# Kernel optimization log

Hardware: AMD Instinct MI355X
Metric: run time of the kernel (lower is better)

The kernel has to match this reference:

```python
import jax, jax.numpy as jnp
import numpy as np

NH = 8          # num_heads
NEG = -1e30     # mask_logits fill value


def setup_inputs() -> dict:
    key = jax.random.key(0)
    k1, k2, k3, k4 = jax.random.split(key, 4)
    B, D, T = 4, 1024, 2048
    x = jax.random.normal(k1, (B, D, T), dtype=jnp.float32)
    mask = jax.random.randint(k2, (B, T), 0, 2).astype(jnp.float32)
    # xavier-uniform-ish linear weights, torch layout [out, in]
    lim = float(np.sqrt(6.0 / (D + D)))
    Wq = jax.random.uniform(k3, (D, D), dtype=jnp.float32, minval=-lim, maxval=lim)
    Wo = jax.random.uniform(k4, (D, D), dtype=jnp.float32, minval=-lim, maxval=lim)
    return {"x": x, "mask": mask, "Wq": Wq, "Wo": Wo}


def reference(x, mask, Wq, Wo):
    # x: [B, D, T] channels-first; mask: [B, T] in {0,1} float
    B, D, T = x.shape
    dk = D // NH
    scale = 1.0 / jnp.sqrt(jnp.asarray(dk, x.dtype))
    xt = jnp.transpose(x, (0, 2, 1))                 # [B, T, D]
    # NOTE: original source uses Wqs for Q, K and V (source bug, reproduced)
    q = xt @ Wq.T                                    # [B, T, D]
    qh = q.reshape(B, T, NH, dk).transpose(0, 2, 1, 3)  # [B, H, T, dk]
    scores = scale * jnp.einsum('bhqd,bhkd->bhqk', qh, qh)  # [B, H, T, T]
    cmask = mask[:, None, None, :]                   # column mask [B,1,1,T]
    rmask = mask[:, None, :, None]                   # row mask    [B,1,T,1]
    logits = (scores * cmask + (1.0 - cmask) * NEG) * rmask
    attn = jax.nn.softmax(logits, axis=-1)
    ctx = jnp.einsum('bhqk,bhkd->bhqd', attn, qh)    # [B, H, T, dk]
    ctx = ctx.transpose(0, 2, 1, 3).reshape(B, T, D)
    out = ctx @ Wo.T                                 # [B, T, D]
    return jnp.transpose(out, (0, 2, 1))             # [B, D, T]
```

## Files before the change

### kernel.cpp

```cpp
#include <hip/hip_runtime.h>

#define TT 2048
#define DD 1024
#define NHH 8
#define DKK 128
#define SCALE2 0.1275174724f

typedef __attribute__((ext_vector_type(8)))  short short8;
typedef __attribute__((ext_vector_type(4)))  short short4v;
typedef __attribute__((ext_vector_type(4)))  float float4v;
typedef __attribute__((ext_vector_type(16))) float float16v;
typedef __attribute__((ext_vector_type(4)))  int   int4v;

__device__ __forceinline__ short f2bf(float f) {
  union { float f; unsigned u; } v; v.f = f;
  unsigned r = v.u + 0x7FFFu + ((v.u >> 16) & 1u);
  return (short)(r >> 16);
}
__device__ __forceinline__ unsigned cvtpk(float lo, float hi) {
  unsigned r;
  asm("v_cvt_pk_bf16_f32 %0, %1, %2" : "=v"(r) : "v"(lo), "v"(hi));
  return r;
}
__device__ __forceinline__ float xhalf_add(float x) {
  float y;
  asm("v_mov_b32 %0, %1" : "=v"(y) : "v"(x));
  asm("v_permlane32_swap_b32 %0, %1" : "+v"(x), "+v"(y));
  return x + y;
}
__device__ __forceinline__ int s4(int row) {
  return (row & 7) ^ (((row >> 3) & 3) << 2);
}
__device__ __forceinline__ void gl2lds(const void* g, void* l) {
  __builtin_amdgcn_global_load_lds(
      (const __attribute__((address_space(1))) void*)g,
      (__attribute__((address_space(3))) void*)l, 16, 0, 0);
}

__global__ __launch_bounds__(256) void k_prep(const float* __restrict__ x,
                                              short* __restrict__ xt,
                                              const float* __restrict__ Wq,
                                              short* __restrict__ wqb,
                                              const float* __restrict__ Wo,
                                              short* __restrict__ wob) {
  int id = blockIdx.x;
  if (id < 8192) {
    __shared__ float tile[32][33];
    int ttile = id & 63, dtile = (id >> 6) & 31, b = id >> 11;
    int d0 = dtile << 5, t0 = ttile << 5;
    int tx = threadIdx.x & 31, ty = threadIdx.x >> 5;
    const float* xp = x + ((size_t)b * DD + d0) * TT + t0;
#pragma unroll
    for (int yy = 0; yy < 32; yy += 8)
      tile[ty + yy][tx] = xp[(size_t)(ty + yy) * TT + tx];
    __syncthreads();
    short* op = xt + ((size_t)b * TT + t0) * DD + d0;
#pragma unroll
    for (int yy = 0; yy < 32; yy += 8)
      op[(size_t)(ty + yy) * DD + tx] = f2bf(tile[tx][ty + yy]);
  } else {
    const float* w = (id < 9216) ? Wq : Wo;
    short* o = (id < 9216) ? wqb : wob;
    int i = (id - 8192 - ((id < 9216) ? 0 : 1024)) * 256 + threadIdx.x;
    float4v v = ((const float4v*)w)[i];
    short4v s;
#pragma unroll
    for (int j = 0; j < 4; ++j) s[j] = f2bf(v[j]);
    ((short4v*)o)[i] = s;
  }
}

template <int EPI>
__global__ __launch_bounds__(256) void k_gemm(const short* __restrict__ A,
                                              const short* __restrict__ Bt,
                                              void* __restrict__ Cout,
                                              short* __restrict__ qhT) {
  __shared__ __align__(16) short As[128 * 64];
  __shared__ __align__(16) short Bs[128 * 64];
  __shared__ __align__(16) short Ct[(EPI == 0) ? 128 * 136 : 1];
  const int K = 1024;
  int tm = blockIdx.x * 128, tn = blockIdx.y * 128;
  int tid = threadIdx.x, lane = tid & 63, w = tid >> 6;
  int wm = (w >> 1) * 64, wn = (w & 1) * 64;
  int ql = lane & 15, g = lane >> 4;

  int srow[4], scol[4];
#pragma unroll
  for (int c = 0; c < 4; ++c) {
    int cg = w * 4 + c;
    int r = cg * 8 + (lane >> 3);
    srow[c] = r;
    scol[c] = ((lane & 7) ^ (r & 7)) * 8;
  }

  float4v acc[4][4];
#pragma unroll
  for (int mt = 0; mt < 4; ++mt)
#pragma unroll
    for (int nt = 0; nt < 4; ++nt) acc[mt][nt] = (float4v){0.f, 0.f, 0.f, 0.f};

  for (int k0 = 0; k0 < K; k0 += 64) {
    __syncthreads();
#pragma unroll
    for (int c = 0; c < 4; ++c) {
      int cg = w * 4 + c;
      gl2lds(A + (size_t)(tm + srow[c]) * K + k0 + scol[c], As + cg * 512);
      gl2lds(Bt + (size_t)(tn + srow[c]) * K + k0 + scol[c], Bs + cg * 512);
    }
    __syncthreads();
#pragma unroll
    for (int k4 = 0; k4 < 2; ++k4) {
      short8 af[4], bfr[4];
#pragma unroll
      for (int mt = 0; mt < 4; ++mt) {
        int row = wm + mt * 16 + ql;
        af[mt] = *(const short8*)(As + row * 64 + (((k4 * 4 + g) ^ (ql & 7)) * 8));
      }
#pragma unroll
      for (int nt = 0; nt < 4; ++nt) {
        int row = wn + nt * 16 + ql;
        bfr[nt] = *(const short8*)(Bs + row * 64 + (((k4 * 4 + g) ^ (ql & 7)) * 8));
      }
#pragma unroll
      for (int mt = 0; mt < 4; ++mt)
#pragma unroll
        for (int nt = 0; nt < 4; ++nt)
          acc[mt][nt] = __builtin_amdgcn_mfma_f32_16x16x32_bf16(af[mt], bfr[nt],
                                                                acc[mt][nt], 0, 0, 0);
    }
  }

  if (EPI == 1) {
#pragma unroll
    for (int mt = 0; mt < 4; ++mt)
#pragma unroll
      for (int nt = 0; nt < 4; ++nt)
#pragma unroll
        for (int r = 0; r < 4; ++r) {
          int m = tm + wm + mt * 16 + g * 4 + r;
          int n = tn + wn + nt * 16 + ql;
          int b = n >> 11, t = n & 2047;
          ((float*)Cout)[((size_t)b * 1024 + m) * 2048 + t] = acc[mt][nt][r];
        }
  } else {
    __syncthreads();
#pragma unroll
    for (int mt = 0; mt < 4; ++mt)
#pragma unroll
      for (int nt = 0; nt < 4; ++nt)
#pragma unroll
        for (int r = 0; r < 4; ++r)
          Ct[(wm + mt * 16 + g * 4 + r) * 136 + wn + nt * 16 + ql] =
              f2bf(acc[mt][nt][r]);
    __syncthreads();
    int bb = tm >> 11, t0 = tm & 2047;
    short* qb = (short*)Cout;
    {
      int m = tid >> 1, c0 = (tid & 1) * 64;
      short* dst = qb + (size_t)(tm + m) * 1024 + tn + c0;
      const short* src = Ct + m * 136 + c0;
#pragma unroll
      for (int i = 0; i < 8; ++i)
        *(short8*)(dst + i * 8) = *(const short8*)(src + i * 8);
    }
    {
      int n = tid >> 1, m0 = (tid & 1) * 64;
      short* dst = qhT + ((size_t)(bb * DD + tn + n)) * TT + t0 + m0;
#pragma unroll
      for (int i = 0; i < 8; ++i) {
        short8 v;
#pragma unroll
        for (int j = 0; j < 8; ++j) v[j] = Ct[(m0 + i * 8 + j) * 136 + n];
        *(short8*)(dst + i * 8) = v;
      }
    }
  }
}

__global__ __launch_bounds__(256, 2) void k_attn(const short* __restrict__ q,
                                                 const short* __restrict__ qhT,
                                                 const float* __restrict__ mask,
                                                 short* __restrict__ ctx) {
  __shared__ __align__(16) short Ks[2][64 * 128];
  __shared__ __align__(16) short Vt[2][128 * 64];
  __shared__ __align__(16) short Kx[2][64 * 16];

  int bh = blockIdx.x, qt = blockIdx.y;
  int b = bh >> 3, h = bh & 7;
  int tid = threadIdx.x, lane = tid & 63, w = tid >> 6;
  int ql32 = lane & 31, hi = lane >> 5;
  int csw = s4(ql32);
  int vsw = ql32 & 7;
  short negbig = f2bf(-1e30f);

  int qrow = qt * 128 + w * 32 + ql32;
  const short* qp = q + ((size_t)(b * TT + qrow)) * DD + h * DKK;
  short8 qf[8];
#pragma unroll
  for (int kc8 = 0; kc8 < 8; ++kc8)
    qf[kc8] = *(const short8*)(qp + kc8 * 16 + hi * 8);
  float rm = mask[(size_t)b * TT + qrow];

  float qs = SCALE2 * rm;
#pragma unroll
  for (int kc8 = 0; kc8 < 8; ++kc8) {
    union { short8 s; unsigned u[4]; } a;
    a.s = qf[kc8];
#pragma unroll
    for (int j = 0; j < 4; ++j) {
      union { unsigned u; float f; } lo, hh;
      lo.u = a.u[j] << 16;
      hh.u = a.u[j] & 0xFFFF0000u;
      a.u[j] = cvtpk(lo.f * qs, hh.f * qs);
    }
    qf[kc8] = a.s;
  }
  short8 bext = (short8)0;
  if (hi == 0) bext[0] = (rm != 0.f) ? (short)0x3F80 : (short)0;

  int oc = tid & 15, r2 = tid >> 4;
  const short* kbase_g = q + ((size_t)b * TT) * DD + h * DKK + oc * 8;
  const short* vbase_g = qhT + ((size_t)(b * DD + h * DKK)) * TT;
  int vd[4], vko[4], vwoff[4];
#pragma unroll
  for (int p = 0; p < 4; ++p) {
    int idx = p * 256 + tid;
    vd[p] = idx >> 3;
    vko[p] = idx & 7;
    vwoff[p] = vd[p] * 64 + ((vko[p] ^ (vd[p] & 7)) * 8);
  }
  int kwoff[2][2];
#pragma unroll
  for (int ps = 0; ps < 2; ++ps) {
    int ra = 2 * r2 + 32 * ps, rb = ra + 1;
    kwoff[ps][0] = ra * 128 + ((oc ^ s4(ra)) * 8);
    kwoff[ps][1] = rb * 128 + ((oc ^ s4(rb)) * 8);
  }

  short8 va[2], vb[2], vv[4];
#pragma unroll
  for (int ps = 0; ps < 2; ++ps) {
    const short* kp = kbase_g + (size_t)(2 * r2 + 32 * ps) * DD;
    va[ps] = *(const short8*)(kp);
    vb[ps] = *(const short8*)(kp + DD);
  }
#pragma unroll
  for (int p = 0; p < 4; ++p)
    vv[p] = *(const short8*)(vbase_g + (size_t)vd[p] * TT + vko[p] * 8);
  float mreg = mask[(size_t)b * TT + lane];

#pragma unroll
  for (int ps = 0; ps < 2; ++ps) {
    *(short8*)(Ks[0] + kwoff[ps][0]) = va[ps];
    *(short8*)(Ks[0] + kwoff[ps][1]) = vb[ps];
  }
#pragma unroll
  for (int p = 0; p < 4; ++p)
    *(short8*)(Vt[0] + vwoff[p]) = vv[p];
  if (tid < 128) {
    short8 z = (short8)0;
    if (tid < 64) z[0] = (mreg != 0.f) ? (short)0 : negbig;
    *(short8*)(&Kx[0][0] + tid * 16) = z;
    *(short8*)(&Kx[0][0] + tid * 16 + 8) = (short8)0;
  }

  float l_run = 0.f;
  float16v o[4];
#pragma unroll
  for (int nt = 0; nt < 4; ++nt)
#pragma unroll
    for (int r = 0; r < 16; ++r) o[nt][r] = 0.f;

  for (int kt = 0; kt < 32; ++kt) {
    int cur = kt & 1;
    const short* ksb = Ks[cur];
    const short* vtb = Vt[cur];
    const short* kxb = Kx[cur];
    short* ksn = Ks[cur ^ 1];
    short* vtn = Vt[cur ^ 1];
    short* kxn = Kx[cur ^ 1];

    __syncthreads();

    if (kt < 31) {
      int kb0n = (kt + 1) * 64;
      const short* kpn = kbase_g + (size_t)kb0n * DD;
#pragma unroll
      for (int ps = 0; ps < 2; ++ps) {
        const short* kp = kpn + (size_t)(2 * r2 + 32 * ps) * DD;
        va[ps] = *(const short8*)(kp);
        vb[ps] = *(const short8*)(kp + DD);
      }
#pragma unroll
      for (int p = 0; p < 4; ++p)
        vv[p] = *(const short8*)(vbase_g + (size_t)vd[p] * TT + kb0n + vko[p] * 8);
      mreg = mask[(size_t)b * TT + kb0n + lane];
    }

    float16v st0, st1;
#pragma unroll
    for (int r = 0; r < 16; ++r) { st0[r] = 0.f; st1[r] = 0.f; }
    __builtin_amdgcn_s_setprio(1);
    {
      short8 ax0 = *(const short8*)(kxb + ql32 * 16 + hi * 8);
      short8 ax1 = *(const short8*)(kxb + (32 + ql32) * 16 + hi * 8);
      st0 = __builtin_amdgcn_mfma_f32_32x32x16_bf16(ax0, bext, st0, 0, 0, 0);
      st1 = __builtin_amdgcn_mfma_f32_32x32x16_bf16(ax1, bext, st1, 0, 0, 0);
    }
#pragma unroll
    for (int kc8 = 0; kc8 < 8; ++kc8) {
      int csk = ((kc8 * 2 + hi) ^ csw) * 8;
      short8 kf0 = *(const short8*)(ksb + ql32 * 128 + csk);
      short8 kf1 = *(const short8*)(ksb + (32 + ql32) * 128 + csk);
      st0 = __builtin_amdgcn_mfma_f32_32x32x16_bf16(kf0, qf[kc8], st0, 0, 0, 0);
      st1 = __builtin_amdgcn_mfma_f32_32x32x16_bf16(kf1, qf[kc8], st1, 0, 0, 0);
    }
    __builtin_amdgcn_s_setprio(0);

    float tsum = 0.f;
#pragma unroll
    for (int r = 0; r < 16; ++r) {
      float p0 = __builtin_amdgcn_exp2f(st0[r]);
      float p1 = __builtin_amdgcn_exp2f(st1[r]);
      st0[r] = p0; st1[r] = p1;
      tsum += p0 + p1;
    }
    l_run += xhalf_add(tsum);

    short8 pa[4];
#pragma unroll
    for (int kc = 0; kc < 4; ++kc) {
      int a0 = 2 * (kc & 1);
      unsigned x0, x1, y0, y1;
      if (kc < 2) {
        x0 = cvtpk(st0[4 * a0 + 0], st0[4 * a0 + 1]);
        x1 = cvtpk(st0[4 * a0 + 2], st0[4 * a0 + 3]);
        y0 = cvtpk(st0[4 * a0 + 4], st0[4 * a0 + 5]);
        y1 = cvtpk(st0[4 * a0 + 6], st0[4 * a0 + 7]);
      } else {
        x0 = cvtpk(st1[4 * a0 + 0], st1[4 * a0 + 1]);
        x1 = cvtpk(st1[4 * a0 + 2], st1[4 * a0 + 3]);
        y0 = cvtpk(st1[4 * a0 + 4], st1[4 * a0 + 5]);
        y1 = cvtpk(st1[4 * a0 + 6], st1[4 * a0 + 7]);
      }
      asm("v_permlane32_swap_b32 %0, %1" : "+v"(x0), "+v"(y0));
      asm("v_permlane32_swap_b32 %0, %1" : "+v"(x1), "+v"(y1));
      union { unsigned u[4]; short8 s8; } pu;
      pu.u[0] = x0; pu.u[1] = x1; pu.u[2] = y0; pu.u[3] = y1;
      pa[kc] = pu.s8;
    }

    __builtin_amdgcn_s_setprio(1);
#pragma unroll
    for (int nt = 0; nt < 4; ++nt) {
      int row = nt * 32 + ql32;
#pragma unroll
      for (int kc = 0; kc < 4; ++kc) {
        short8 vf = *(const short8*)(vtb + row * 64 + (((kc * 2 + hi) ^ vsw) * 8));
        o[nt] = __builtin_amdgcn_mfma_f32_32x32x16_bf16(vf, pa[kc], o[nt], 0, 0, 0);
      }
    }
    __builtin_amdgcn_s_setprio(0);

    if (kt < 31) {
#pragma unroll
      for (int ps = 0; ps < 2; ++ps) {
        *(short8*)(ksn + kwoff[ps][0]) = va[ps];
        *(short8*)(ksn + kwoff[ps][1]) = vb[ps];
      }
#pragma unroll
      for (int p = 0; p < 4; ++p)
        *(short8*)(vtn + vwoff[p]) = vv[p];
      if (tid < 64) {
        unsigned word = (mreg != 0.f) ? 0u : (unsigned)(unsigned short)negbig;
        *(unsigned*)(kxn + tid * 16) = word;
      }
    }
  }

  float il = 1.0f / l_run;
  short* cp = ctx + ((size_t)(b * TT + qrow)) * DD + h * DKK;
#pragma unroll
  for (int nt = 0; nt < 4; ++nt)
#pragma unroll
    for (int a = 0; a < 4; ++a) {
      short4v sv;
#pragma unroll
      for (int j = 0; j < 4; ++j) sv[j] = f2bf(o[nt][4 * a + j] * il);
      *(short4v*)(cp + nt * 32 + 8 * a + 4 * hi) = sv;
    }
}

extern "C" void kernel_launch(void* const* d_in, const int* in_sizes, int n_in,
                              void* d_out, int out_size, void* d_ws, size_t ws_size,
                              hipStream_t stream) {
  const float* x    = (const float*)d_in[0];
  const float* mask = (const float*)d_in[1];
  const float* Wq   = (const float*)d_in[2];
  const float* Wo   = (const float*)d_in[3];
  char* ws = (char*)d_ws;
  short* xt  = (short*)(ws);
  short* wqb = (short*)(ws + (size_t)16 * 1024 * 1024);
  short* wob = (short*)(ws + (size_t)18 * 1024 * 1024);
  short* qb  = (short*)(ws + (size_t)20 * 1024 * 1024);
  short* ctx = (short*)(ws + (size_t)36 * 1024 * 1024);
  short* qhT = (short*)(ws + (size_t)52 * 1024 * 1024);

  k_prep<<<10240, 256, 0, stream>>>(x, xt, Wq, wqb, Wo, wob);
  k_gemm<0><<<dim3(64, 8), 256, 0, stream>>>(xt, wqb, qb, qhT);
  k_attn<<<dim3(32, 16), 256, 0, stream>>>(qb, qhT, mask, ctx);
  k_gemm<1><<<dim3(8, 64), 256, 0, stream>>>(wob, ctx, d_out, nullptr);
}
```

Baseline: 145.7 us.

## Split attention KV range across two wave groups per block and merge partials

The attention kernel now launches 512 threads per block, split into two 256-thread groups. Each group handles half of the key/value sequence for the same 128 query rows, and the two partial outputs and row sums are merged through shared memory at the end. The LDS double-buffering is replaced by single buffers per group with two barriers per iteration. The goal is more waves in flight, since the grid of 512 blocks underfills the device, at the cost of extra synchronization, a shared-memory reduction, and possibly lower occupancy from the larger LDS footprint and register pressure.

```diff
diff --git a/kernel.cpp b/kernel.cpp
--- a/kernel.cpp
+++ b/kernel.cpp
@@ -177,23 +177,34 @@
   }
 }
 
-__global__ __launch_bounds__(256, 2) void k_attn(const short* __restrict__ q,
+__global__ __launch_bounds__(512, 4) void k_attn(const short* __restrict__ q,
                                                  const short* __restrict__ qhT,
                                                  const float* __restrict__ mask,
                                                  short* __restrict__ ctx) {
-  __shared__ __align__(16) short Ks[2][64 * 128];
-  __shared__ __align__(16) short Vt[2][128 * 64];
-  __shared__ __align__(16) short Kx[2][64 * 16];
+  __shared__ __align__(16) char smem[69632];
+  short* KsAll = (short*)smem;
+  short* VtAll = (short*)(smem + 32768);
+  short* KxAll = (short*)(smem + 65536);
+  float* Obf = (float*)smem;
+  float* lb  = (float*)(smem + 67584);
 
   int bh = blockIdx.x, qt = blockIdx.y;
   int b = bh >> 3, h = bh & 7;
-  int tid = threadIdx.x, lane = tid & 63, w = tid >> 6;
+  int tid = threadIdx.x;
+  int g = tid >> 8;
+  int gtid = tid & 255;
+  int lane = tid & 63;
+  int w4 = gtid >> 6;
   int ql32 = lane & 31, hi = lane >> 5;
   int csw = s4(ql32);
   int vsw = ql32 & 7;
   short negbig = f2bf(-1e30f);
 
-  int qrow = qt * 128 + w * 32 + ql32;
+  short* Ks_g = KsAll + g * 8192;
+  short* Vt_g = VtAll + g * 8192;
+  short* Kx_g = KxAll + g * 1024;
+
+  int qrow = qt * 128 + w4 * 32 + ql32;
   const short* qp = q + ((size_t)(b * TT + qrow)) * DD + h * DKK;
   short8 qf[8];
 #pragma unroll
@@ -218,13 +229,13 @@
   short8 bext = (short8)0;
   if (hi == 0) bext[0] = (rm != 0.f) ? (short)0x3F80 : (short)0;
 
-  int oc = tid & 15, r2 = tid >> 4;
+  int oc = gtid & 15, r2 = gtid >> 4;
   const short* kbase_g = q + ((size_t)b * TT) * DD + h * DKK + oc * 8;
   const short* vbase_g = qhT + ((size_t)(b * DD + h * DKK)) * TT;
   int vd[4], vko[4], vwoff[4];
 #pragma unroll
   for (int p = 0; p < 4; ++p) {
-    int idx = p * 256 + tid;
+    int idx = p * 256 + gtid;
     vd[p] = idx >> 3;
     vko[p] = idx & 7;
     vwoff[p] = vd[p] * 64 + ((vko[p] ^ (vd[p] & 7)) * 8);
@@ -237,31 +248,26 @@
     kwoff[ps][1] = rb * 128 + ((oc ^ s4(rb)) * 8);
   }
 
+  int kv0 = g * 16;
+
   short8 va[2], vb[2], vv[4];
-#pragma unroll
-  for (int ps = 0; ps < 2; ++ps) {
-    const short* kp = kbase_g + (size_t)(2 * r2 + 32 * ps) * DD;
-    va[ps] = *(const short8*)(kp);
-    vb[ps] = *(const short8*)(kp + DD);
-  }
-#pragma unroll
-  for (int p = 0; p < 4; ++p)
-    vv[p] = *(const short8*)(vbase_g + (size_t)vd[p] * TT + vko[p] * 8);
-  float mreg = mask[(size_t)b * TT + lane];
-
-#pragma unroll
-  for (int ps = 0; ps < 2; ++ps) {
-    *(short8*)(Ks[0] + kwoff[ps][0]) = va[ps];
-    *(short8*)(Ks[0] + kwoff[ps][1]) = vb[ps];
-  }
-#pragma unroll
-  for (int p = 0; p < 4; ++p)
-    *(short8*)(Vt[0] + vwoff[p]) = vv[p];
-  if (tid < 128) {
-    short8 z = (short8)0;
-    if (tid < 64) z[0] = (mreg != 0.f) ? (short)0 : negbig;
-    *(short8*)(&Kx[0][0] + tid * 16) = z;
-    *(short8*)(&Kx[0][0] + tid * 16 + 8) = (short8)0;
+  {
+    int kb0 = kv0 * 64;
+    const short* kp0 = kbase_g + (size_t)kb0 * DD;
+#pragma unroll
+    for (int ps = 0; ps < 2; ++ps) {
+      const short* kp = kp0 + (size_t)(2 * r2 + 32 * ps) * DD;
+      va[ps] = *(const short8*)(kp);
+      vb[ps] = *(const short8*)(kp + DD);
+    }
+#pragma unroll
+    for (int p = 0; p < 4; ++p)
+      vv[p] = *(const short8*)(vbase_g + (size_t)vd[p] * TT + kb0 + vko[p] * 8);
+  }
+  float mreg = mask[(size_t)b * TT + kv0 * 64 + lane];
+  if (gtid < 64) {
+    *(short8*)(Kx_g + gtid * 16) = (short8)0;
+    *(short8*)(Kx_g + gtid * 16 + 8) = (short8)0;
   }
 
   float l_run = 0.f;
@@ -271,19 +277,25 @@
 #pragma unroll
     for (int r = 0; r < 16; ++r) o[nt][r] = 0.f;
 
-  for (int kt = 0; kt < 32; ++kt) {
-    int cur = kt & 1;
-    const short* ksb = Ks[cur];
-    const short* vtb = Vt[cur];
-    const short* kxb = Kx[cur];
-    short* ksn = Ks[cur ^ 1];
-    short* vtn = Vt[cur ^ 1];
-    short* kxn = Kx[cur ^ 1];
-
-    __syncthreads();
-
-    if (kt < 31) {
-      int kb0n = (kt + 1) * 64;
+  for (int it = 0; it < 16; ++it) {
+    __syncthreads();
+
+#pragma unroll
+    for (int ps = 0; ps < 2; ++ps) {
+      *(short8*)(Ks_g + kwoff[ps][0]) = va[ps];
+      *(short8*)(Ks_g + kwoff[ps][1]) = vb[ps];
+    }
+#pragma unroll
+    for (int p = 0; p < 4; ++p)
+      *(short8*)(Vt_g + vwoff[p]) = vv[p];
+    if (gtid < 64) {
+      unsigned word = (mreg != 0.f) ? 0u : (unsigned)(unsigned short)negbig;
+      *(unsigned*)(Kx_g + gtid * 16) = word;
+    }
+    __syncthreads();
+
+    if (it < 15) {
+      int kb0n = (kv0 + it + 1) * 64;
       const short* kpn = kbase_g + (size_t)kb0n * DD;
 #pragma unroll
       for (int ps = 0; ps < 2; ++ps) {
@@ -302,16 +314,16 @@
     for (int r = 0; r < 16; ++r) { st0[r] = 0.f; st1[r] = 0.f; }
     __builtin_amdgcn_s_setprio(1);
     {
-      short8 ax0 = *(const short8*)(kxb + ql32 * 16 + hi * 8);
-      short8 ax1 = *(const short8*)(kxb + (32 + ql32) * 16 + hi * 8);
+      short8 ax0 = *(const short8*)(Kx_g + ql32 * 16 + hi * 8);
+      short8 ax1 = *(const short8*)(Kx_g + (32 + ql32) * 16 + hi * 8);
       st0 = __builtin_amdgcn_mfma_f32_32x32x16_bf16(ax0, bext, st0, 0, 0, 0);
       st1 = __builtin_amdgcn_mfma_f32_32x32x16_bf16(ax1, bext, st1, 0, 0, 0);
     }
 #pragma unroll
     for (int kc8 = 0; kc8 < 8; ++kc8) {
       int csk = ((kc8 * 2 + hi) ^ csw) * 8;
-      short8 kf0 = *(const short8*)(ksb + ql32 * 128 + csk);
-      short8 kf1 = *(const short8*)(ksb + (32 + ql32) * 128 + csk);
+      short8 kf0 = *(const short8*)(Ks_g + ql32 * 128 + csk);
+      short8 kf1 = *(const short8*)(Ks_g + (32 + ql32) * 128 + csk);
       st0 = __builtin_amdgcn_mfma_f32_32x32x16_bf16(kf0, qf[kc8], st0, 0, 0, 0);
       st1 = __builtin_amdgcn_mfma_f32_32x32x16_bf16(kf1, qf[kc8], st1, 0, 0, 0);
     }
@@ -356,39 +368,43 @@
       int row = nt * 32 + ql32;
 #pragma unroll
       for (int kc = 0; kc < 4; ++kc) {
-        short8 vf = *(const short8*)(vtb + row * 64 + (((kc * 2 + hi) ^ vsw) * 8));
+        short8 vf = *(const short8*)(Vt_g + row * 64 + (((kc * 2 + hi) ^ vsw) * 8));
         o[nt] = __builtin_amdgcn_mfma_f32_32x32x16_bf16(vf, pa[kc], o[nt], 0, 0, 0);
       }
     }
     __builtin_amdgcn_s_setprio(0);
-
-    if (kt < 31) {
-#pragma unroll
-      for (int ps = 0; ps < 2; ++ps) {
-        *(short8*)(ksn + kwoff[ps][0]) = va[ps];
-        *(short8*)(ksn + kwoff[ps][1]) = vb[ps];
-      }
-#pragma unroll
-      for (int p = 0; p < 4; ++p)
-        *(short8*)(vtn + vwoff[p]) = vv[p];
-      if (tid < 64) {
-        unsigned word = (mreg != 0.f) ? 0u : (unsigned)(unsigned short)negbig;
-        *(unsigned*)(kxn + tid * 16) = word;
-      }
-    }
-  }
-
-  float il = 1.0f / l_run;
-  short* cp = ctx + ((size_t)(b * TT + qrow)) * DD + h * DKK;
-#pragma unroll
-  for (int nt = 0; nt < 4; ++nt)
-#pragma unroll
-    for (int a = 0; a < 4; ++a) {
-      short4v sv;
-#pragma unroll
-      for (int j = 0; j < 4; ++j) sv[j] = f2bf(o[nt][4 * a + j] * il);
-      *(short4v*)(cp + nt * 32 + 8 * a + 4 * hi) = sv;
-    }
+  }
+
+  __syncthreads();
+  int qc = w4 * 32 + ql32;
+  if (g == 1) {
+#pragma unroll
+    for (int nt = 0; nt < 4; ++nt)
+#pragma unroll
+      for (int a = 0; a < 4; ++a) {
+        float4v t;
+#pragma unroll
+        for (int j = 0; j < 4; ++j) t[j] = o[nt][4 * a + j];
+        *(float4v*)(&Obf[qc * 132 + nt * 32 + 8 * a + 4 * hi]) = t;
+      }
+    if (hi == 0) lb[qc] = l_run;
+  }
+  __syncthreads();
+  if (g == 0) {
+    l_run += lb[qc];
+    float il = 1.0f / l_run;
+    short* cp = ctx + ((size_t)(b * TT + qrow)) * DD + h * DKK;
+#pragma unroll
+    for (int nt = 0; nt < 4; ++nt)
+#pragma unroll
+      for (int a = 0; a < 4; ++a) {
+        float4v t = *(const float4v*)(&Obf[qc * 132 + nt * 32 + 8 * a + 4 * hi]);
+        short4v sv;
+#pragma unroll
+        for (int j = 0; j < 4; ++j) sv[j] = f2bf((o[nt][4 * a + j] + t[j]) * il);
+        *(short4v*)(cp + nt * 32 + 8 * a + 4 * hi) = sv;
+      }
+  }
 }
 
 extern "C" void kernel_launch(void* const* d_in, const int* in_sizes, int n_in,
@@ -408,6 +424,6 @@
 
   k_prep<<<10240, 256, 0, stream>>>(x, xt, Wq, wqb, Wo, wob);
   k_gemm<0><<<dim3(64, 8), 256, 0, stream>>>(xt, wqb, qb, qhT);
-  k_attn<<<dim3(32, 16), 256, 0, stream>>>(qb, qhT, mask, ctx);
+  k_attn<<<dim3(32, 16), 512, 0, stream>>>(qb, qhT, mask, ctx);
   k_gemm<1><<<dim3(8, 64), 256, 0, stream>>>(wob, ctx, d_out, nullptr);
 }
```

After: 349.2 us. 2.4x slower.
